# Kernel optimization log

Hardware: AMD Instinct MI355X
Metric: run time of the kernel (lower is better)

## Reference

```python
import jax, jax.numpy as jnp
import numpy as np

BETA = 0.9      # leak factor of snn.Leaky
THR = 1.0       # default threshold

# snntorch surrogate.atan(): forward = Heaviside(U), backward = (alpha/2)/(1+(pi/2*alpha*U)^2) with alpha=2 -> 1/(1+(pi*U)^2)
@jax.custom_vjp
def atan_spike(u):
    return (u > 0).astype(u.dtype)

def _atan_fwd(u):
    return atan_spike(u), u

def _atan_bwd(u, g):
    return (g / (1.0 + (jnp.pi * u) ** 2),)

atan_spike.defvjp(_atan_fwd, _atan_bwd)


def setup_inputs() -> dict:
    key = jax.random.key(0)
    k0, k1, k2 = jax.random.split(key, 3)
    T, B, H, W = 50, 128, 128, 128
    ni, nh, no = H * W, 256, 11
    x = jax.random.normal(k0, (T, B, H, W), dtype=jnp.float32)
    W1 = jax.random.normal(k1, (nh, ni), dtype=jnp.float32) / np.sqrt(ni).astype(np.float32)
    b1 = jnp.zeros((nh,), jnp.float32)
    W2 = jax.random.normal(k2, (no, nh), dtype=jnp.float32) / np.sqrt(nh).astype(np.float32)
    b2 = jnpphantom = None
    b2 = jnp.zeros((no,), jnp.float32)
    return {"x": x, "W1": W1, "b1": b1, "W2": W2, "b2": b2}


def reference(x, W1, b1, W2, b2):
    T, B = x.shape[0], x.shape[1]
    xf = x.reshape(T, B, -1)  # [T, B, 16384]

    def step(carry, xt):
        mem1, mem2 = carry
        cur1 = xt @ W1.T + b1                       # [B, nh]
        mem1 = BETA * mem1 + cur1
        spk1 = atan_spike(mem1 - THR)
        mem1 = mem1 - jax.lax.stop_gradient(spk1) * THR  # subtract reset (detached, as in snntorch)
        cur2 = spk1 @ W2.T + b2                     # [B, no]
        mem2 = BETA * mem2 + cur2
        spk2 = atan_spike(mem2 - THR)
        mem2 = mem2 - jax.lax.stop_gradient(spk2) * THR
        return (mem1, mem2), spk2

    mem1_0 = jnp.zeros((B, W1.shape[0]), x.dtype)
    mem2_0 = jnp.zeros((B, W2.shape[0]), x.dtype)
    _, spk2_rec = jax.lax.scan(step, (mem1_0, mem2_0), xf)
    return spk2_rec  # [T, B, 11]
```

## Files before the change

### kernel.cpp

```cpp
#include <hip/hip_runtime.h>


#define T_STEPS 50
#define BATCH   128
#define NI      16384
#define NH      256
#define NO      11
#define M_TOT   (T_STEPS * BATCH)
#define KSPLIT  8
#define KCHUNK  (NI / KSPLIT)
#define BK      32
#define KTILES  (KCHUNK / BK)
#define BM      128
#define BN      256

typedef _Float16 f16x8 __attribute__((ext_vector_type(8)));
typedef _Float16 f16x4 __attribute__((ext_vector_type(4)));
typedef float    f32x4 __attribute__((ext_vector_type(4)));

__device__ __forceinline__ void split2(float f, _Float16& hi, _Float16& lo) {
    hi = (_Float16)f;
    lo = (_Float16)(f - (float)hi);
}

__device__ __forceinline__ int swz(int row, int blk) {
    return row * BK + ((blk ^ ((row >> 1) & 3)) << 3);
}

typedef __attribute__((address_space(1))) const unsigned int guint;
typedef __attribute__((address_space(3))) unsigned int luint;
__device__ __forceinline__ void lds16(const void* g, void* l) {
    __builtin_amdgcn_global_load_lds((guint*)g, (luint*)l, 16, 0, 0);
}

__global__ __launch_bounds__(256) void convert_w1(
    const float* __restrict__ W1, _Float16* __restrict__ Wh, _Float16* __restrict__ Wl)
{
    const size_t i = ((size_t)blockIdx.x * 256 + threadIdx.x) * 4;
    const float4 v = *(const float4*)(W1 + i);
    float a[4] = { v.x, v.y, v.z, v.w };
    f16x4 h, l;
#pragma unroll
    for (int j = 0; j < 4; ++j) {
        _Float16 hh, ll;
        split2(a[j], hh, ll);
        h[j] = hh; l[j] = ll;
    }
    *(f16x4*)(Wh + i) = h;
    *(f16x4*)(Wl + i) = l;
}

__global__ __launch_bounds__(256, 2) void gemm1_mfma(
    const float* __restrict__ X, const _Float16* __restrict__ W1h,
    const _Float16* __restrict__ W1l, float* __restrict__ part)
{
    __shared__ alignas(16) _Float16 Ah[BM * BK];
    __shared__ alignas(16) _Float16 Al[BM * BK];
    __shared__ alignas(16) _Float16 Bh[BN * BK];
    __shared__ alignas(16) _Float16 Bl[BN * BK];

    const int tid  = threadIdx.x;
    const int lane = tid & 63;
    const int wave = tid >> 6;
    const int wm   = wave >> 1;
    const int wn   = wave & 1;
    const int q    = lane >> 4;
    const int l15  = lane & 15;

    const int m0 = blockIdx.x * BM;
    const int ks = blockIdx.y;
    const int kbase = ks * KCHUNK;

    const int a_row[2] = { tid >> 2, 64 + (tid >> 2) };
    const int a_g8     = tid & 3;

    int b_row[4], b_fb[4];
#pragma unroll
    for (int j = 0; j < 4; ++j) {
        b_row[j] = wave * 64 + j * 16 + (lane >> 2);
        b_fb[j]  = (lane & 3) ^ ((b_row[j] >> 1) & 3);
    }

    f32x4 acc[4][8];
#pragma unroll
    for (int im = 0; im < 4; ++im)
#pragma unroll
        for (int jn = 0; jn < 8; ++jn) acc[im][jn] = (f32x4){0.f, 0.f, 0.f, 0.f};

    const int xsw = (l15 >> 1) & 3;
    const int qx  = (q ^ xsw) << 3;

    for (int kt = 0; kt < KTILES; ++kt) {
        const int k0 = kbase + kt * BK;

        f16x8 ahv[2], alv[2];
#pragma unroll
        for (int i = 0; i < 2; ++i) {
            const float* s = X + (size_t)(m0 + a_row[i]) * NI + k0 + a_g8 * 8;
            const float4 v0 = *(const float4*)s, v1 = *(const float4*)(s + 4);
            float av[8] = { v0.x, v0.y, v0.z, v0.w, v1.x, v1.y, v1.z, v1.w };
#pragma unroll
            for (int j = 0; j < 8; ++j) { _Float16 h, l; split2(av[j], h, l); ahv[i][j] = h; alv[i][j] = l; }
        }

        __syncthreads();

#pragma unroll
        for (int j = 0; j < 4; ++j) {
            const size_t goff = (size_t)b_row[j] * NI + k0 + b_fb[j] * 8;
            const int lbase = (wave * 4 + j) * 512;
            lds16(W1h + goff, &Bh[lbase]);
            lds16(W1l + goff, &Bl[lbase]);
        }

#pragma unroll
        for (int i = 0; i < 2; ++i) {
            const int off = swz(a_row[i], a_g8);
            *(f16x8*)&Ah[off] = ahv[i];
            *(f16x8*)&Al[off] = alv[i];
        }

        __syncthreads();

        f16x8 fah[4], fal[4];
#pragma unroll
        for (int im = 0; im < 4; ++im) {
            const int off = (64 * wm + 16 * im + l15) * BK + qx;
            fah[im] = *(const f16x8*)&Ah[off];
            fal[im] = *(const f16x8*)&Al[off];
        }
#pragma unroll
        for (int jn = 0; jn < 8; ++jn) {
            const int off = (128 * wn + 16 * jn + l15) * BK + qx;
            const f16x8 fbh = *(const f16x8*)&Bh[off];
            const f16x8 fbl = *(const f16x8*)&Bl[off];
#pragma unroll
            for (int im = 0; im < 4; ++im) {
                acc[im][jn] = __builtin_amdgcn_mfma_f32_16x16x32_f16(fah[im], fbh, acc[im][jn], 0, 0, 0);
                acc[im][jn] = __builtin_amdgcn_mfma_f32_16x16x32_f16(fal[im], fbh, acc[im][jn], 0, 0, 0);
                acc[im][jn] = __builtin_amdgcn_mfma_f32_16x16x32_f16(fah[im], fbl, acc[im][jn], 0, 0, 0);
            }
        }
    }

    float* P = part + (size_t)ks * M_TOT * NH;
#pragma unroll
    for (int im = 0; im < 4; ++im) {
        const int mrow = m0 + 64 * wm + 16 * im + 4 * q;
#pragma unroll
        for (int jn = 0; jn < 8; ++jn) {
            const int n = 128 * wn + 16 * jn + l15;
#pragma unroll
            for (int r = 0; r < 4; ++r)
                P[(size_t)(mrow + r) * NH + n] = acc[im][jn][r];
        }
    }
}

__global__ __launch_bounds__(256) void scan1_kernel(
    const float* __restrict__ part, const float* __restrict__ b1,
    float* __restrict__ spk1)
{
    const int b = blockIdx.x;
    const int h = threadIdx.x;
    const float bias = b1[h];
    const size_t S = (size_t)M_TOT * NH;
    float mem = 0.f;
    for (int t = 0; t < T_STEPS; ++t) {
        const size_t idx = ((size_t)(t * BATCH + b)) * NH + h;
        float c = ((part[idx] + part[S + idx]) + (part[2 * S + idx] + part[3 * S + idx]))
                + ((part[4 * S + idx] + part[5 * S + idx]) + (part[6 * S + idx] + part[7 * S + idx]));
        c += bias;
        mem = __fadd_rn(__fmul_rn(0.9f, mem), c);
        const float s = (mem > 1.0f) ? 1.0f : 0.0f;
        mem -= s;
        spk1[idx] = s;
    }
}

__global__ __launch_bounds__(256) void gemm2_kernel(
    const float* __restrict__ spk1, const float* __restrict__ W2,
    const float* __restrict__ b2, float* __restrict__ cur2)
{
    const int wave = threadIdx.x >> 6;
    const int lane = threadIdx.x & 63;
    const int m = blockIdx.x * 4 + wave;
    const float4 s4 = *(const float4*)(spk1 + (size_t)m * NH + (lane << 2));
#pragma unroll
    for (int o = 0; o < NO; ++o) {
        const float4 w4 = *(const float4*)(W2 + (size_t)o * NH + (lane << 2));
        float p = (s4.x * w4.x + s4.y * w4.y) + (s4.z * w4.z + s4.w * w4.w);
#pragma unroll
        for (int d = 32; d; d >>= 1) p += __shfl_xor(p, d, 64);
        if (lane == 0) cur2[(size_t)m * 16 + o] = p + b2[o];
    }
}

__global__ __launch_bounds__(256) void scan2_kernel(
    const float* __restrict__ cur2, float* __restrict__ out)
{
    const int tid = blockIdx.x * 256 + threadIdx.x;
    if (tid >= BATCH * NO) return;
    const int b = tid / NO, o = tid % NO;
    float mem = 0.f;
    for (int t = 0; t < T_STEPS; ++t) {
        const float c = cur2[(size_t)(t * BATCH + b) * 16 + o];
        mem = __fadd_rn(__fmul_rn(0.9f, mem), c);
        const float s = (mem > 1.0f) ? 1.0f : 0.0f;
        mem -= s;
        out[(size_t)(t * BATCH + b) * NO + o] = s;
    }
}

extern "C" void kernel_launch(void* const* d_in, const int* in_sizes, int n_in,
                              void* d_out, int out_size, void* d_ws, size_t ws_size,
                              hipStream_t stream) {
    const float* x  = (const float*)d_in[0];
    const float* W1 = (const float*)d_in[1];
    const float* b1 = (const float*)d_in[2];
    const float* W2 = (const float*)d_in[3];
    const float* b2 = (const float*)d_in[4];
    float* out = (float*)d_out;

    float* part = (float*)d_ws;
    float* spk1 = part + (size_t)KSPLIT * M_TOT * NH;
    float* cur2 = spk1 + (size_t)M_TOT * NH;
    _Float16* W1h = (_Float16*)(cur2 + (size_t)M_TOT * 16);
    _Float16* W1l = W1h + (size_t)NH * NI;

    convert_w1<<<(NH * NI) / (256 * 4), 256, 0, stream>>>(W1, W1h, W1l);
    dim3 g1(M_TOT / BM, KSPLIT);
    gemm1_mfma<<<g1, 256, 0, stream>>>(x, W1h, W1l, part);
    scan1_kernel<<<BATCH, NH, 0, stream>>>(part, b1, spk1);
    gemm2_kernel<<<M_TOT / 4, 256, 0, stream>>>(spk1, W2, b2, cur2);
    scan2_kernel<<<(BATCH * NO + 255) / 256, 256, 0, stream>>>(cur2, out);
}
```

Baseline: 674.7 us.

## Fuse layer-1 scan, layer-2 matvec and layer-2 scan into one tail kernel

Replaces the three tail kernels (scan1, gemm2, scan2) with a single per-batch kernel. It keeps layer-1 spikes in shared memory, computes the 11 output currents with wave reductions against W2 staged in LDS, and runs the layer-2 membrane recurrence in registers. It also prefetches the next timestep's eight split-K partials while the current step is processed. This removes two kernel launches and the spk1/cur2 global round trips, at the cost of two block barriers per timestep on only 128 blocks.

```diff
diff --git a/kernel.cpp b/kernel.cpp
--- a/kernel.cpp
+++ b/kernel.cpp
@@ -157,58 +157,81 @@
     }
 }
 
-__global__ __launch_bounds__(256) void scan1_kernel(
+__global__ __launch_bounds__(256) void fused_tail(
     const float* __restrict__ part, const float* __restrict__ b1,
-    float* __restrict__ spk1)
+    const float* __restrict__ W2, const float* __restrict__ b2,
+    float* __restrict__ out)
 {
-    const int b = blockIdx.x;
-    const int h = threadIdx.x;
+    __shared__ float sp[NH];
+    __shared__ float w2s[NO * NH];
+
+    const int b    = blockIdx.x;
+    const int h    = threadIdx.x;
+    const int wave = h >> 6;
+    const int lane = h & 63;
+
+    for (int i = h; i < NO * NH; i += 256) w2s[i] = W2[i];
+
     const float bias = b1[h];
     const size_t S = (size_t)M_TOT * NH;
-    float mem = 0.f;
+
+    float mem2[3] = {0.f, 0.f, 0.f};
+    float bias2[3];
+#pragma unroll
+    for (int oi = 0; oi < 3; ++oi) {
+        const int o = wave + 4 * oi;
+        bias2[oi] = (o < NO) ? b2[o] : 0.f;
+    }
+
+    float mem1 = 0.f;
+    float c8[8], cn8[8];
+
+    {
+        const size_t idx = (size_t)b * NH + h;
+#pragma unroll
+        for (int ksi = 0; ksi < 8; ++ksi) c8[ksi] = part[ksi * S + idx];
+    }
+
+    __syncthreads();
+
     for (int t = 0; t < T_STEPS; ++t) {
-        const size_t idx = ((size_t)(t * BATCH + b)) * NH + h;
-        float c = ((part[idx] + part[S + idx]) + (part[2 * S + idx] + part[3 * S + idx]))
-                + ((part[4 * S + idx] + part[5 * S + idx]) + (part[6 * S + idx] + part[7 * S + idx]));
+        if (t + 1 < T_STEPS) {
+            const size_t idx = ((size_t)((t + 1) * BATCH + b)) * NH + h;
+#pragma unroll
+            for (int ksi = 0; ksi < 8; ++ksi) cn8[ksi] = part[ksi * S + idx];
+        }
+
+        float c = ((c8[0] + c8[1]) + (c8[2] + c8[3]))
+                + ((c8[4] + c8[5]) + (c8[6] + c8[7]));
         c += bias;
-        mem = __fadd_rn(__fmul_rn(0.9f, mem), c);
-        const float s = (mem > 1.0f) ? 1.0f : 0.0f;
-        mem -= s;
-        spk1[idx] = s;
-    }
-}
-
-__global__ __launch_bounds__(256) void gemm2_kernel(
-    const float* __restrict__ spk1, const float* __restrict__ W2,
-    const float* __restrict__ b2, float* __restrict__ cur2)
-{
-    const int wave = threadIdx.x >> 6;
-    const int lane = threadIdx.x & 63;
-    const int m = blockIdx.x * 4 + wave;
-    const float4 s4 = *(const float4*)(spk1 + (size_t)m * NH + (lane << 2));
-#pragma unroll
-    for (int o = 0; o < NO; ++o) {
-        const float4 w4 = *(const float4*)(W2 + (size_t)o * NH + (lane << 2));
-        float p = (s4.x * w4.x + s4.y * w4.y) + (s4.z * w4.z + s4.w * w4.w);
-#pragma unroll
-        for (int d = 32; d; d >>= 1) p += __shfl_xor(p, d, 64);
-        if (lane == 0) cur2[(size_t)m * 16 + o] = p + b2[o];
-    }
-}
-
-__global__ __launch_bounds__(256) void scan2_kernel(
-    const float* __restrict__ cur2, float* __restrict__ out)
-{
-    const int tid = blockIdx.x * 256 + threadIdx.x;
-    if (tid >= BATCH * NO) return;
-    const int b = tid / NO, o = tid % NO;
-    float mem = 0.f;
-    for (int t = 0; t < T_STEPS; ++t) {
-        const float c = cur2[(size_t)(t * BATCH + b) * 16 + o];
-        mem = __fadd_rn(__fmul_rn(0.9f, mem), c);
-        const float s = (mem > 1.0f) ? 1.0f : 0.0f;
-        mem -= s;
-        out[(size_t)(t * BATCH + b) * NO + o] = s;
+        mem1 = __fadd_rn(__fmul_rn(0.9f, mem1), c);
+        const float s1 = (mem1 > 1.0f) ? 1.0f : 0.0f;
+        mem1 -= s1;
+        sp[h] = s1;
+
+        __syncthreads();
+
+        const float4 s4 = *(const float4*)&sp[lane << 2];
+#pragma unroll
+        for (int oi = 0; oi < 3; ++oi) {
+            const int o = wave + 4 * oi;
+            if (o < NO) {
+                const float4 w4 = *(const float4*)&w2s[o * NH + (lane << 2)];
+                float p = (s4.x * w4.x + s4.y * w4.y) + (s4.z * w4.z + s4.w * w4.w);
+#pragma unroll
+                for (int d = 32; d; d >>= 1) p += __shfl_xor(p, d, 64);
+                const float c2 = p + bias2[oi];
+                mem2[oi] = __fadd_rn(__fmul_rn(0.9f, mem2[oi]), c2);
+                const float s2 = (mem2[oi] > 1.0f) ? 1.0f : 0.0f;
+                mem2[oi] -= s2;
+                if (lane == 0) out[(size_t)(t * BATCH + b) * NO + o] = s2;
+            }
+        }
+
+        __syncthreads();
+
+#pragma unroll
+        for (int ksi = 0; ksi < 8; ++ksi) c8[ksi] = cn8[ksi];
     }
 }
 
@@ -223,15 +246,11 @@
     float* out = (float*)d_out;
 
     float* part = (float*)d_ws;
-    float* spk1 = part + (size_t)KSPLIT * M_TOT * NH;
-    float* cur2 = spk1 + (size_t)M_TOT * NH;
-    _Float16* W1h = (_Float16*)(cur2 + (size_t)M_TOT * 16);
+    _Float16* W1h = (_Float16*)(part + (size_t)KSPLIT * M_TOT * NH);
     _Float16* W1l = W1h + (size_t)NH * NI;
 
     convert_w1<<<(NH * NI) / (256 * 4), 256, 0, stream>>>(W1, W1h, W1l);
     dim3 g1(M_TOT / BM, KSPLIT);
     gemm1_mfma<<<g1, 256, 0, stream>>>(x, W1h, W1l, part);
-    scan1_kernel<<<BATCH, NH, 0, stream>>>(part, b1, spk1);
-    gemm2_kernel<<<M_TOT / 4, 256, 0, stream>>>(spk1, W2, b2, cur2);
-    scan2_kernel<<<(BATCH * NO + 255) / 256, 256, 0, stream>>>(cur2, out);
-}
+    fused_tail<<<BATCH, NH, 0, stream>>>(part, b1, W2, b2, out);
+}
```

New measurement: 697.2 us. +3.3%, slower.
